# Kernel tuning notes

Hardware: AMD Instinct MI355X
Metric: run time of the kernel (lower is better)

Reference implementation:

```python
import jax, jax.numpy as jnp
import numpy as np

T, V, C, G = 65536, 25, 3, 3
H = 32        # GCN hidden channels
OUT = 8       # cfg.STGCN.OUT_FEATURES
LH = 8        # LSTM hidden
DH = 64       # discriminator hidden


def setup_inputs() -> dict:
    key = jax.random.key(0)
    ks = jax.random.split(key, 16)
    def n(i, shape, s=0.3):
        return jax.random.normal(ks[i], shape, dtype=jnp.float32) * s
    A = jax.random.uniform(ks[0], (V, V), dtype=jnp.float32)
    A = A / A.sum(axis=1, keepdims=True)  # row-normalized adjacency
    return dict(
        x=jax.random.normal(ks[1], (1, C, T, V, G), dtype=jnp.float32),
        x0=jax.random.normal(ks[2], (1, 2), dtype=jnp.float32),
        A=A,
        W1=n(3, (H, C)), b1=jnp.zeros((H,), jnp.float32),
        W2=n(4, (OUT, H)), b2=jnp.zeros((OUT,), jnp.float32),
        Wih0=n(5, (4 * LH, 2)), Whh0=n(6, (4 * LH, LH)),
        bih0=jnp.zeros((4 * LH,), jnp.float32), bhh0=jnp.zeros((4 * LH,), jnp.float32),
        Wih1=n(7, (4 * LH, LH)), Whh1=n(8, (4 * LH, LH)),
        bih1=jnp.zeros((4 * LH,), jnp.float32), bhh1=jnp.zeros((4 * LH,), jnp.float32),
        Wfc1=n(9, (8, 32)), bfc1=jnp.zeros((8,), jnp.float32),
        Wfc2=n(10, (2, 8)), bfc2=jnp.zeros((2,), jnp.float32),
        Wd1=n(11, (DH, 32)), bd1=jnp.zeros((DH,), jnp.float32),
        Wd2=n(12, (1, DH)), bd2=jnp.zeros((1,), jnp.float32),
    )


def reference(x, x0, A, W1, b1, W2, b2,
              Wih0, Whh0, bih0, bhh0, Wih1, Whh1, bih1, bhh1,
              Wfc1, bfc1, Wfc2, bfc2, Wd1, bd1, Wd2, bd2):
    Tn = x.shape[2]
    # --- ST-GCN on every (t, group) slice, vectorized over time ---
    g = jnp.transpose(x[0], (1, 3, 0, 2))                       # [T,G,C,V]
    agg = jnp.einsum('tgcv,vu->tgcu', g, A)                     # graph aggregation
    hid = jax.nn.relu(jnp.einsum('hc,tgcu->tghu', W1, agg)
                      + b1[None, None, :, None])                # [T,G,H,V]
    pooled = hid.mean(axis=-1)                                  # global joint pool [T,G,H]
    gout = (jnp.einsum('oh,tgh->tgo', W2, pooled) + b2).reshape(Tn, G * OUT)  # [T,24]
    # --- circle through the 3 group members (joint 5, channels 0/2), faithful formula ---
    px = x[0, 0, :, 5, :]                                       # [T,3]
    py = x[0, 2, :, 5, :]
    x21 = px[:, 1] - px[:, 0]; y21 = py[:, 1] - py[:, 0]
    x32 = px[:, 2] - px[:, 1]; y32 = py[:, 2] - py[:, 1]
    xy21 = px[:, 1] ** 2 - px[:, 0] ** 2 + py[:, 1] ** 2 - py[:, 0] ** 2
    xy32 = px[:, 2] ** 2 - px[:, 1] ** 2 + py[:, 2] ** 2 - py[:, 1] ** 2
    cy = (x32 * xy21 - x21 * xy32) / 2 * (y21 * x32 - y32 * x21)
    cx = (xy21 - 2 * cy * y21) / (2.0 * x21)
    cr = jnp.sqrt((px[:, 0] - cx) ** 2 + (py[:, 0] - cy) ** 2)

    def lstm_cell(inp, h, c, Wih, Whh, bih, bhh):
        gates = Wih @ inp + bih + Whh @ h + bhh
        i, f, gg, o = jnp.split(gates, 4)
        c2 = jax.nn.sigmoid(f) * c + jax.nn.sigmoid(i) * jnp.tanh(gg)
        return jax.nn.sigmoid(o) * jnp.tanh(c2), c2

    # Re-running the LSTM from zero init over the growing traj and taking the last
    # output (as the torch code does) == stepping the LSTM incrementally.
    def step(carry, xs):
        h0, c0, h1, c1, pt = carry
        go, rx, ry, rr = xs
        h0, c0 = lstm_cell(pt, h0, c0, Wih0, Whh0, bih0, bhh0)
        h1, c1 = lstm_cell(h0, h1, c1, Wih1, Whh1, bih1, bhh1)
        state = jnp.concatenate([h1, go])                       # [32]
        reward = jax.nn.sigmoid(Wd2 @ jnp.tanh(Wd1 @ state + bd1) + bd2)
        nxt = Wfc2 @ (Wfc1 @ state + bfc1) + bfc2               # [2]
        dis = jnp.sqrt((nxt[0] - rx) ** 2 + (nxt[1] - ry) ** 2)
        mask = (dis < rr).astype(jnp.int32)
        return (h0, c0, h1, c1, nxt), (state, nxt, reward, mask)

    z = jnp.zeros((LH,), jnp.float32)
    carry0 = (z, z, z, z, x0.reshape(2))
    xs = (gout[:Tn - 1], cx[:Tn - 1], cy[:Tn - 1], cr[:Tn - 1])
    _, (states, nxts, rewards, masks) = jax.lax.scan(step, carry0, xs)
    traj = jnp.concatenate([x0.reshape(1, 2), nxts], axis=0)    # [T,2]
    return states, traj, rewards, masks
```

## Files before the change

kernel.cpp:

```cpp
#include <hip/hip_runtime.h>
#include <math.h>

#define TT 65536
#define NS 65535
#define VV 25
#define CC 3
#define GG 3
#define HH 32
#define OO 8

#define CHUNK 32
#define NCHUNK 2048
#define WARM 96

#define OFF_WC    0
#define OFF_BC    64
#define OFF_W0H1  128
#define OFF_PSCAN 512

#define OUT_STATES 0
#define OUT_TRAJ   (NS*32)
#define OUT_REW    (OUT_TRAJ + TT*2)
#define OUT_MASK   (OUT_REW + NS)

__device__ __forceinline__ float fsigm(float x){ return 1.0f/(1.0f+__expf(-x)); }
__device__ __forceinline__ float ftanh(float x){ return 2.0f/(1.0f+__expf(-2.0f*x)) - 1.0f; }

#define QP(x, k) __int_as_float(__builtin_amdgcn_update_dpp(0, __float_as_int(x), (k)*0x55, 0xF, 0xF, true))
#define RDL(x, l) __int_as_float(__builtin_amdgcn_readlane(__float_as_int(x), (l)))

__device__ __forceinline__ void pkfma_s(float2& acc, float2 w, float2 h){
  asm("v_pk_fma_f32 %0, %1, %2, %0" : "+v"(acc) : "v"(w), "s"(h));
}
__device__ __forceinline__ void pkmul_s(float2& d, float2 w, float2 h){
  asm("v_pk_mul_f32 %0, %1, %2" : "=v"(d) : "v"(w), "s"(h));
}
__device__ __forceinline__ void pkfma_sv(float2& d, float2 w, float2 p, float2 add){
  asm("v_pk_fma_f32 %0, %1, %2, %3" : "=v"(d) : "v"(w), "s"(p), "v"(add));
}
__device__ __forceinline__ float2 pkadd_v(float2 a, float2 b){
  float2 d; asm("v_pk_add_f32 %0, %1, %2" : "=v"(d) : "v"(a), "v"(b)); return d;
}

__global__ __launch_bounds__(64) void kW(const float* __restrict__ Wfc1, const float* __restrict__ bfc1,
    const float* __restrict__ Wfc2, const float* __restrict__ bfc2,
    const float* __restrict__ Wih0, const float* __restrict__ x0, float* __restrict__ ws)
{
  __shared__ float WcL[64];
  int t = threadIdx.x;
  int o = t >> 5, k = t & 31;
  float acc = 0.f;
  #pragma unroll
  for (int m = 0; m < 8; ++m) acc += Wfc2[o*8+m]*Wfc1[m*32+k];
  WcL[t] = acc;
  ws[OFF_WC + t] = acc;
  if (t < 2){
    float b = bfc2[t];
    #pragma unroll
    for (int m = 0; m < 8; ++m) b += Wfc2[t*8+m]*bfc1[m];
    ws[OFF_BC + t] = b;
    ws[OFF_PSCAN + t] = x0[t];
  }
  __syncthreads();
  #pragma unroll
  for (int q = 0; q < 4; ++q){
    int idx = t + 64*q;
    int gg = idx >> 3, jj = idx & 7;
    ws[OFF_W0H1 + idx] = Wih0[gg*2+0]*WcL[jj] + Wih0[gg*2+1]*WcL[32+jj];
  }
}

__global__ __launch_bounds__(192) void kGCN(const float* __restrict__ x, const float* __restrict__ A,
    const float* __restrict__ W1, const float* __restrict__ b1,
    const float* __restrict__ W2, const float* __restrict__ b2,
    float* __restrict__ ws, float* __restrict__ out)
{
  __shared__ __align__(16) float xs[64*75];
  __shared__ float goL[192][8];
  const int tid = threadIdx.x;
  const int t0 = blockIdx.x * 64;
  const int dt = tid / 3, g = tid - 3*dt;
  const int t = t0 + dt;

  float xg[CC][VV];
  #pragma unroll
  for (int c = 0; c < CC; ++c){
    if (c) __syncthreads();
    const float4* sc = (const float4*)(x + ((size_t)c*TT + t0)*75);
    float4* dd = (float4*)xs;
    for (int i = tid; i < 1200; i += 192) dd[i] = sc[i];
    __syncthreads();
    const float* bp = xs + dt*75 + g;
    #pragma unroll
    for (int v = 0; v < VV; ++v) xg[c][v] = bp[v*3];
  }

  float pooled[HH];
  #pragma unroll
  for (int h = 0; h < HH; ++h) pooled[h] = 0.f;

  for (int u = 0; u < VV; ++u){
    float a0 = 0.f, a1 = 0.f, a2 = 0.f;
    #pragma unroll
    for (int v = 0; v < VV; ++v){
      float Av = A[v*VV + u];
      a0 += xg[0][v]*Av; a1 += xg[1][v]*Av; a2 += xg[2][v]*Av;
    }
    #pragma unroll
    for (int h = 0; h < HH; ++h){
      float hv = W1[h*3+0]*a0 + W1[h*3+1]*a1 + W1[h*3+2]*a2 + b1[h];
      pooled[h] += fmaxf(hv, 0.f);
    }
  }

  if (t < NS){
    float pm[HH];
    #pragma unroll
    for (int h = 0; h < HH; ++h) pm[h] = pooled[h]*(1.0f/VV);
    #pragma unroll
    for (int o = 0; o < OO; ++o){
      float go = b2[o];
      #pragma unroll
      for (int h = 0; h < HH; ++h) go += W2[o*HH+h]*pm[h];
      out[(size_t)t*32 + 8 + g*8 + o] = go;
      goL[tid][o] = go;
    }
  }
  __syncthreads();

  if (tid < 64){
    int tt = t0 + tid;
    if (tt < NS-1){
      float p0 = ws[OFF_BC+0], p1 = ws[OFF_BC+1];
      #pragma unroll
      for (int k = 0; k < 24; ++k){
        float gk = goL[tid*3 + (k>>3)][k&7];
        p0 += ws[OFF_WC + 8 + k]  * gk;
        p1 += ws[OFF_WC + 40 + k] * gk;
      }
      ws[OFF_PSCAN + 2*(tt+1) + 0] = p0;
      ws[OFF_PSCAN + 2*(tt+1) + 1] = p1;
    }
  }
}

__global__ __launch_bounds__(64) void kScan(const float* __restrict__ ws,
    const float* __restrict__ Wih0, const float* __restrict__ Whh0,
    const float* __restrict__ bih0, const float* __restrict__ bhh0,
    const float* __restrict__ Wih1, const float* __restrict__ Whh1,
    const float* __restrict__ bih1, const float* __restrict__ bhh1,
    float* __restrict__ out)
{
  const int lane = threadIdx.x & 63;
  const int row  = lane & 3;
  const int cell = (lane >> 2) & 7;
  const int G    = row*8 + cell;
  const bool up  = lane >= 32;
  const bool isT = (row == 2);

  const float L2E = 1.4426950408889634f;
  const float nsc = isT ? -2.0f*L2E : -L2E;
  const float k2  = -2.0f*L2E;

  float2 wA[4], wB[4], wP, bP;
  #pragma unroll
  for (int q = 0; q < 4; ++q){
    if (up){
      wA[q].x = nsc*Whh1[G*8 + 2*q];  wA[q].y = nsc*Whh1[G*8 + 2*q+1];
      wB[q].x = nsc*Wih1[G*8 + 2*q];  wB[q].y = nsc*Wih1[G*8 + 2*q+1];
    } else {
      wA[q].x = nsc*ws[OFF_W0H1 + G*8 + 2*q];  wA[q].y = nsc*ws[OFF_W0H1 + G*8 + 2*q+1];
      wB[q].x = nsc*Whh0[G*8 + 2*q];           wB[q].y = nsc*Whh0[G*8 + 2*q+1];
    }
  }
  if (up){ wP.x = 0.f; wP.y = 0.f; bP.x = nsc*(bih1[G] + bhh1[G]); }
  else   { wP.x = nsc*Wih0[G*2+0]; wP.y = nsc*Wih0[G*2+1]; bP.x = nsc*(bih0[G] + bhh0[G]); }
  bP.y = 0.f;

  float cs0 = 0.f, cs1 = 0.f;
  float Dprev = 0.f;
  float2 hp1[4], hp0[4];
  #pragma unroll
  for (int q = 0; q < 4; ++q){ hp1[q].x = 0.f; hp1[q].y = 0.f; hp0[q].x = 0.f; hp0[q].y = 0.f; }

  const float2* Ps = (const float2*)(ws + OFF_PSCAN);
  const bool doStore = up && (row == 0);

  auto STEP = [&](float2 P) -> float {
    float2 accP;
    pkfma_sv(accP, wP, P, bP);
    float2 xa = accP;
    pkfma_s(xa, wA[0], hp1[0]);
    float2 ya;
    pkmul_s(ya, wA[1], hp1[1]);
    pkfma_s(xa, wA[2], hp1[2]);
    pkfma_s(ya, wA[3], hp1[3]);
    float2 sA = pkadd_v(xa, ya);
    float dotA = sA.x + sA.y;
    float gA = dotA + Dprev;

    float e0 = __builtin_amdgcn_exp2f(gA);
    float r0 = __builtin_amdgcn_rcpf(1.0f + e0);
    float iv = QP(r0, 0), fv = QP(r0, 1), gvr = QP(r0, 2), ov = QP(r0, 3);
    float gvc = __builtin_fmaf(gvr, 2.0f*k2, -k2);
    cs0 = __builtin_fmaf(fv, cs0, iv*gvc);
    float ec = __builtin_amdgcn_exp2f(cs0);
    float rc = __builtin_amdgcn_rcpf(1.0f + ec);
    float h0v = __builtin_fmaf(rc, ov + ov, -ov);

    #pragma unroll
    for (int q = 0; q < 4; ++q){ hp0[q].x = RDL(h0v, 8*q); hp0[q].y = RDL(h0v, 8*q + 4); }

    float2 xb, yb;
    pkmul_s(xb, wB[0], hp0[0]);
    pkmul_s(yb, wB[1], hp0[1]);
    pkfma_s(xb, wB[2], hp0[2]);
    pkfma_s(yb, wB[3], hp0[3]);
    float2 sB = pkadd_v(xb, yb);
    float dotB = sB.x + sB.y;
    float gB = dotB + dotA;

    float e1 = __builtin_amdgcn_exp2f(gB);
    float r1 = __builtin_amdgcn_rcpf(1.0f + e1);
    float iw = QP(r1, 0), fw = QP(r1, 1), gwr = QP(r1, 2), ow = QP(r1, 3);
    float gwc = __builtin_fmaf(gwr, 2.0f*k2, -k2);
    cs1 = __builtin_fmaf(fw, cs1, iw*gwc);
    float ed = __builtin_amdgcn_exp2f(cs1);
    float rd = __builtin_amdgcn_rcpf(1.0f + ed);
    float h1v = __builtin_fmaf(rd, ow + ow, -ow);

    #pragma unroll
    for (int q = 0; q < 4; ++q){ hp1[q].x = RDL(h1v, 32 + 8*q); hp1[q].y = RDL(h1v, 32 + 8*q + 4); }

    Dprev = dotB;
    return h1v;
  };

  const int ck   = blockIdx.x;
  const int s0   = ck * CHUNK;
  const int sBeg = (s0 > WARM) ? (s0 - WARM) : 0;
  const int sEnd = (s0 + CHUNK > NS) ? NS : (s0 + CHUNK);
  float* op = out + (size_t)s0*32;

  float2 cur[8], nxt[8];

  if (s0 > sBeg){
    #pragma unroll
    for (int u = 0; u < 8; ++u) cur[u] = Ps[sBeg + u];
    for (int blk = sBeg; blk < s0; blk += 8){
      #pragma unroll
      for (int u = 0; u < 8; ++u){ int ix = blk + 8 + u; nxt[u] = Ps[ix < NS ? ix : NS-1]; }
      #pragma unroll
      for (int u = 0; u < 8; ++u) STEP(cur[u]);
      #pragma unroll
      for (int u = 0; u < 8; ++u) cur[u] = nxt[u];
    }
  }

  {
    const int len   = sEnd - s0;
    const int nfull = len & ~7;
    #pragma unroll
    for (int u = 0; u < 8; ++u){ int ix = s0 + u; cur[u] = Ps[ix < NS ? ix : NS-1]; }
    for (int blk = s0; blk < s0 + nfull; blk += 8){
      #pragma unroll
      for (int u = 0; u < 8; ++u){ int ix = blk + 8 + u; nxt[u] = Ps[ix < NS ? ix : NS-1]; }
      #pragma unroll
      for (int u = 0; u < 8; ++u){
        float h = STEP(cur[u]);
        if (doStore) op[cell] = h;
        op += 32;
      }
      #pragma unroll
      for (int u = 0; u < 8; ++u) cur[u] = nxt[u];
    }
    for (int s = s0 + nfull; s < sEnd; ++s){
      float h = STEP(Ps[s]);
      if (doStore) op[cell] = h;
      op += 32;
    }
  }
}

__global__ __launch_bounds__(256) void kPost(const float* __restrict__ x,
    const float* __restrict__ x0, const float* __restrict__ ws,
    const float* __restrict__ Wd1, const float* __restrict__ bd1,
    const float* __restrict__ Wd2, const float* __restrict__ bd2,
    float* __restrict__ out)
{
  __shared__ float Wd1L[64*32];
  __shared__ float bd1L[64], Wd2L[64], WcLs[64], bcL[2];
  int tid = threadIdx.x;
  for (int i = tid; i < 2048; i += 256) Wd1L[i] = Wd1[i];
  if (tid < 64){ bd1L[tid] = bd1[tid]; Wd2L[tid] = Wd2[tid]; WcLs[tid] = ws[OFF_WC + tid]; }
  if (tid < 2) bcL[tid] = ws[OFF_BC + tid];
  __syncthreads();

  int s = blockIdx.x*256 + tid;
  if (s >= NS) return;

  const float4* rp = (const float4*)(out + (size_t)s*32);
  float st[32];
  #pragma unroll
  for (int q = 0; q < 8; ++q){
    float4 v = rp[q];
    st[4*q] = v.x; st[4*q+1] = v.y; st[4*q+2] = v.z; st[4*q+3] = v.w;
  }
  float n0 = bcL[0], n1 = bcL[1];
  #pragma unroll
  for (int k = 0; k < 32; ++k){ n0 += WcLs[k]*st[k]; n1 += WcLs[32+k]*st[k]; }
  out[OUT_TRAJ + 2*(s+1) + 0] = n0;
  out[OUT_TRAJ + 2*(s+1) + 1] = n1;
  if (s == 0){ out[OUT_TRAJ + 0] = x0[0]; out[OUT_TRAJ + 1] = x0[1]; }

  float accr = bd2[0];
  for (int d = 0; d < 64; ++d){
    float v = bd1L[d];
    #pragma unroll
    for (int k = 0; k < 32; ++k) v += Wd1L[d*32+k]*st[k];
    accr += Wd2L[d]*ftanh(v);
  }
  out[OUT_REW + s] = fsigm(accr);

  float px0 = x[(size_t)s*75 + 15 + 0];
  float px1 = x[(size_t)s*75 + 15 + 1];
  float px2 = x[(size_t)s*75 + 15 + 2];
  const float* py = x + (size_t)2*TT*75;
  float py0 = py[(size_t)s*75 + 15 + 0];
  float py1 = py[(size_t)s*75 + 15 + 1];
  float py2 = py[(size_t)s*75 + 15 + 2];
  float x21 = px1-px0, y21 = py1-py0;
  float x32 = px2-px1, y32 = py2-py1;
  float xy21 = px1*px1 - px0*px0 + py1*py1 - py0*py0;
  float xy32 = px2*px2 - px1*px1 + py2*py2 - py1*py1;
  float cyv = (x32*xy21 - x21*xy32)*0.5f * (y21*x32 - y32*x21);
  float cxv = (xy21 - 2.0f*cyv*y21) / (2.0f*x21);
  float crv = sqrtf((px0-cxv)*(px0-cxv) + (py0-cyv)*(py0-cyv));
  float dx = n0 - cxv, dy = n1 - cyv;
  float dis = sqrtf(dx*dx + dy*dy);
  out[OUT_MASK + s] = (dis < crv) ? 1.0f : 0.0f;
}

extern "C" void kernel_launch(void* const* d_in, const int* in_sizes, int n_in,
                              void* d_out, int out_size, void* d_ws, size_t ws_size,
                              hipStream_t stream) {
  (void)in_sizes; (void)n_in; (void)out_size; (void)ws_size;
  const float* x    = (const float*)d_in[0];
  const float* x0   = (const float*)d_in[1];
  const float* A    = (const float*)d_in[2];
  const float* W1   = (const float*)d_in[3];
  const float* b1   = (const float*)d_in[4];
  const float* W2   = (const float*)d_in[5];
  const float* b2   = (const float*)d_in[6];
  const float* Wih0 = (const float*)d_in[7];
  const float* Whh0 = (const float*)d_in[8];
  const float* bih0 = (const float*)d_in[9];
  const float* bhh0 = (const float*)d_in[10];
  const float* Wih1 = (const float*)d_in[11];
  const float* Whh1 = (const float*)d_in[12];
  const float* bih1 = (const float*)d_in[13];
  const float* bhh1 = (const float*)d_in[14];
  const float* Wfc1 = (const float*)d_in[15];
  const float* bfc1 = (const float*)d_in[16];
  const float* Wfc2 = (const float*)d_in[17];
  const float* bfc2 = (const float*)d_in[18];
  const float* Wd1  = (const float*)d_in[19];
  const float* bd1  = (const float*)d_in[20];
  const float* Wd2  = (const float*)d_in[21];
  const float* bd2  = (const float*)d_in[22];
  float* out = (float*)d_out;
  float* ws  = (float*)d_ws;

  kW   <<<dim3(1),      dim3(64),  0, stream>>>(Wfc1, bfc1, Wfc2, bfc2, Wih0, x0, ws);
  kGCN <<<dim3(1024),   dim3(192), 0, stream>>>(x, A, W1, b1, W2, b2, ws, out);
  kScan<<<dim3(NCHUNK), dim3(64),  0, stream>>>(ws, Wih0, Whh0, bih0, bhh0, Wih1, Whh1, bih1, bhh1, out);
  kPost<<<dim3(256),    dim3(256), 0, stream>>>(x, x0, ws, Wd1, bd1, Wd2, bd2, out);
}
```

Before: 123.7 us.

## Restructure GCN kernel with packed FMA, precomputed transposes, and reduced scan warmup

Precomputes transposed adjacency and W1 into the workspace in kW. kGCN then computes the graph aggregation with packed float2 FMAs, stores the aggregates in LDS, and runs the hidden ReLU-pool stage with packed math over halves of H. It also lowers the scan warm-up length from 96 to 64 steps, which shortens the redundant recurrence per chunk but risks accuracy if the LSTM state has not converged from the warm start. The larger LDS buffer may reduce occupancy.

```diff
diff --git a/kernel.cpp b/kernel.cpp
--- a/kernel.cpp
+++ b/kernel.cpp
@@ -11,12 +11,14 @@
 
 #define CHUNK 32
 #define NCHUNK 2048
-#define WARM 96
+#define WARM 64
 
 #define OFF_WC    0
 #define OFF_BC    64
 #define OFF_W0H1  128
-#define OFF_PSCAN 512
+#define OFF_W1T   384
+#define OFF_AT    512
+#define OFF_PSCAN 1280
 
 #define OUT_STATES 0
 #define OUT_TRAJ   (NS*32)
@@ -41,10 +43,20 @@
 __device__ __forceinline__ float2 pkadd_v(float2 a, float2 b){
   float2 d; asm("v_pk_add_f32 %0, %1, %2" : "=v"(d) : "v"(a), "v"(b)); return d;
 }
+__device__ __forceinline__ void pkmul_vv(float2& d, float2 a, float2 b){
+  asm("v_pk_mul_f32 %0, %1, %2" : "=v"(d) : "v"(a), "v"(b));
+}
+__device__ __forceinline__ void pkfma_vv(float2& acc, float2 a, float2 b){
+  asm("v_pk_fma_f32 %0, %1, %2, %0" : "+v"(acc) : "v"(a), "v"(b));
+}
+__device__ __forceinline__ void pkadd_acc(float2& acc, float2 b){
+  asm("v_pk_add_f32 %0, %0, %1" : "+v"(acc) : "v"(b));
+}
 
 __global__ __launch_bounds__(64) void kW(const float* __restrict__ Wfc1, const float* __restrict__ bfc1,
     const float* __restrict__ Wfc2, const float* __restrict__ bfc2,
-    const float* __restrict__ Wih0, const float* __restrict__ x0, float* __restrict__ ws)
+    const float* __restrict__ Wih0, const float* __restrict__ x0,
+    const float* __restrict__ A, const float* __restrict__ W1, float* __restrict__ ws)
 {
   __shared__ float WcL[64];
   int t = threadIdx.x;
@@ -61,6 +73,14 @@
     ws[OFF_BC + t] = b;
     ws[OFF_PSCAN + t] = x0[t];
   }
+  for (int i = t; i < 26*25; i += 64){
+    int u = i / 26, v = i - 26*u;
+    ws[OFF_AT + i] = (v < 25) ? A[v*25 + u] : 0.f;
+  }
+  for (int i = t; i < 96; i += 64){
+    int c = i >> 5, h = i & 31;
+    ws[OFF_W1T + i] = W1[h*3 + c];
+  }
   __syncthreads();
   #pragma unroll
   for (int q = 0; q < 4; ++q){
@@ -70,53 +90,87 @@
   }
 }
 
-__global__ __launch_bounds__(192) void kGCN(const float* __restrict__ x, const float* __restrict__ A,
-    const float* __restrict__ W1, const float* __restrict__ b1,
-    const float* __restrict__ W2, const float* __restrict__ b2,
+__global__ __launch_bounds__(192) void kGCN(const float* __restrict__ x,
+    const float* __restrict__ b1, const float* __restrict__ W2, const float* __restrict__ b2,
     float* __restrict__ ws, float* __restrict__ out)
 {
-  __shared__ __align__(16) float xs[64*75];
+  __shared__ __align__(16) float smem[192*79];
   __shared__ float goL[192][8];
   const int tid = threadIdx.x;
   const int t0 = blockIdx.x * 64;
   const int dt = tid / 3, g = tid - 3*dt;
   const int t = t0 + dt;
 
-  float xg[CC][VV];
+  float2 xp[3][13];
   #pragma unroll
   for (int c = 0; c < CC; ++c){
     if (c) __syncthreads();
     const float4* sc = (const float4*)(x + ((size_t)c*TT + t0)*75);
-    float4* dd = (float4*)xs;
+    float4* dd = (float4*)smem;
     for (int i = tid; i < 1200; i += 192) dd[i] = sc[i];
     __syncthreads();
-    const float* bp = xs + dt*75 + g;
-    #pragma unroll
-    for (int v = 0; v < VV; ++v) xg[c][v] = bp[v*3];
-  }
-
-  float pooled[HH];
-  #pragma unroll
-  for (int h = 0; h < HH; ++h) pooled[h] = 0.f;
-
+    const float* bp = smem + dt*75 + g;
+    #pragma unroll
+    for (int k = 0; k < 12; ++k){ xp[c][k].x = bp[6*k]; xp[c][k].y = bp[6*k+3]; }
+    xp[c][12].x = bp[72]; xp[c][12].y = 0.f;
+  }
+  __syncthreads();
+
+  float* auL = smem + tid*79;
   for (int u = 0; u < VV; ++u){
-    float a0 = 0.f, a1 = 0.f, a2 = 0.f;
-    #pragma unroll
-    for (int v = 0; v < VV; ++v){
-      float Av = A[v*VV + u];
-      a0 += xg[0][v]*Av; a1 += xg[1][v]*Av; a2 += xg[2][v]*Av;
-    }
-    #pragma unroll
-    for (int h = 0; h < HH; ++h){
-      float hv = W1[h*3+0]*a0 + W1[h*3+1]*a1 + W1[h*3+2]*a2 + b1[h];
-      pooled[h] += fmaxf(hv, 0.f);
-    }
+    const float2* Ap = (const float2*)(ws + OFF_AT + u*26);
+    float a24 = ws[OFF_AT + u*26 + 24];
+    #pragma unroll
+    for (int c = 0; c < CC; ++c){
+      float2 acc;
+      float2 ap = Ap[0];
+      pkmul_vv(acc, xp[c][0], ap);
+      #pragma unroll
+      for (int k = 1; k < 12; ++k){ float2 apk = Ap[k]; pkfma_vv(acc, xp[c][k], apk); }
+      auL[c*26 + u] = __builtin_fmaf(xp[c][12].x, a24, acc.x + acc.y);
+    }
+  }
+
+  const float2* b1g = (const float2*)b1;
+  float2 pooled[16];
+  #pragma unroll
+  for (int half = 0; half < 2; ++half){
+    float2 w1p[3][8], b1p[8], pp[8];
+    #pragma unroll
+    for (int j = 0; j < 8; ++j){
+      b1p[j] = b1g[half*8 + j];
+      #pragma unroll
+      for (int c = 0; c < 3; ++c)
+        w1p[c][j] = *(const float2*)(ws + OFF_W1T + c*32 + half*16 + 2*j);
+      pp[j].x = 0.f; pp[j].y = 0.f;
+    }
+    for (int u = 0; u < VV; ++u){
+      float a0 = auL[u], a1 = auL[26 + u], a2 = auL[52 + u];
+      float2 a0d; a0d.x = a0; a0d.y = a0;
+      float2 a1d; a1d.x = a1; a1d.y = a1;
+      float2 a2d; a2d.x = a2; a2d.y = a2;
+      #pragma unroll
+      for (int j = 0; j < 8; ++j){
+        float2 hv = b1p[j];
+        pkfma_vv(hv, w1p[0][j], a0d);
+        pkfma_vv(hv, w1p[1][j], a1d);
+        pkfma_vv(hv, w1p[2][j], a2d);
+        hv.x = fmaxf(hv.x, 0.f);
+        hv.y = fmaxf(hv.y, 0.f);
+        pkadd_acc(pp[j], hv);
+      }
+    }
+    #pragma unroll
+    for (int j = 0; j < 8; ++j) pooled[half*8 + j] = pp[j];
   }
 
   if (t < NS){
     float pm[HH];
     #pragma unroll
-    for (int h = 0; h < HH; ++h) pm[h] = pooled[h]*(1.0f/VV);
+    for (int h = 0; h < HH; ++h){
+      float ph = (h & 1) ? pooled[h >> 1].y : pooled[h >> 1].x;
+      pm[h] = ph * (1.0f/VV);
+    }
     #pragma unroll
     for (int o = 0; o < OO; ++o){
       float go = b2[o];
@@ -371,8 +425,8 @@
   float* out = (float*)d_out;
   float* ws  = (float*)d_ws;
 
-  kW   <<<dim3(1),      dim3(64),  0, stream>>>(Wfc1, bfc1, Wfc2, bfc2, Wih0, x0, ws);
-  kGCN <<<dim3(1024),   dim3(192), 0, stream>>>(x, A, W1, b1, W2, b2, ws, out);
+  kW   <<<dim3(1),      dim3(64),  0, stream>>>(Wfc1, bfc1, Wfc2, bfc2, Wih0, x0, A, W1, ws);
+  kGCN <<<dim3(1024),   dim3(192), 0, stream>>>(x, b1, W2, b2, ws, out);
   kScan<<<dim3(NCHUNK), dim3(64),  0, stream>>>(ws, Wih0, Whh0, bih0, bhh0, Wih1, Whh1, bih1, bhh1, out);
   kPost<<<dim3(256),    dim3(256), 0, stream>>>(x, x0, ws, Wd1, bd1, Wd2, bd2, out);
 }
```

Result: slower. 132.6 us (+7.2%).
